# Performance work log

Measured on AMD Instinct MI355X. Metric: run time of the kernel, lower is better.

Reference implementation:

```python
import jax, jax.numpy as jnp
import numpy as np

N, L = 5, 2097152
WIDTH = 11  # max_pool1d kernel width in the original


def setup_inputs() -> dict:
    key = jax.random.key(0)
    k1, k2 = jax.random.split(key)
    rppg = jax.random.normal(k1, (N, L), dtype=jnp.float32)
    ppg = jax.random.normal(k2, (N, L), dtype=jnp.float32)
    return {"rppg": rppg, "ppg": ppg, "fs": 30, "epoch": 15}


def _normalize(x):
    # normalize_torch: per-signal standardization
    mu = x.mean(axis=1, keepdims=True)
    sd = x.std(axis=1, keepdims=True)
    return (x - mu) / sd


def _window_max(x, width):
    # sliding max over centered window of `width`, same padding (-inf pad)
    return jax.lax.reduce_window(x, -jnp.inf, jax.lax.max,
                                 (1, width), (1, 1),
                                 [(0, 0), (width // 2, width // 2)])


def _mean_hr(x, fs):
    # A position p is a 'nice peak' iff max_pool argmax at p equals p,
    # i.e. x[p] is the max of its own centered window (ties have measure 0
    # for continuous signals). unique()+masking collapses to this mask.
    w = _window_max(x, WIDTH)
    m1 = x == w                                            # [N, L] peak mask
    npk = m1.sum(axis=1, keepdims=True).astype(x.dtype)
    mean_pk = (x * m1).sum(axis=1, keepdims=True) / npk    # mean of peak values
    m = m1 & (x > mean_pk / 2)                             # amplitude-filtered peaks
    idx = jnp.arange(x.shape[1])
    vals = jnp.where(m, idx, -1)
    # previous peak index strictly before p (fixed-shape replacement for diff
    # over a variable-length peak index list)
    prev = jnp.pad(jax.lax.cummax(vals, axis=1)[:, :-1], ((0, 0), (1, 0)),
                   constant_values=-1)
    valid = m & (prev >= 0)                                # one entry per inter-peak gap
    gaps = (idx[None, :] - prev).astype(x.dtype)
    inv = jnp.where(valid, 1.0 / gaps, 0.0)
    # mean(60 / (gap / fs)) = 60 * fs * mean(1 / gap)
    return (60.0 * fs) * inv.sum(axis=1) / valid.sum(axis=1).astype(x.dtype)


def reference(rppg, ppg, fs, epoch):
    ppg = _normalize(ppg.reshape(N, -1))
    rppg = _normalize(rppg.reshape(N, -1))
    ppg_hr = _mean_hr(ppg, fs)
    rppg_hr = _mean_hr(rppg, fs)
    # hr_score = mean_i |ppg_hr - rppg_hr| / ppg_hr  (peak_score is computed
    # in the original but not returned)
    return jnp.mean(jnp.abs(ppg_hr - rppg_hr) / ppg_hr)
```

## Files before the change

kernel.cpp:

```cpp
#include <hip/hip_runtime.h>
#include <math.h>

namespace {

constexpr int LNUM = 2097152;
constexpr int NROW = 5;
constexpr int NSER = 10;
constexpr int TPB = 256;
constexpr int EPL = 16;
constexpr int CHUNK = TPB * EPL;
constexpr int CPR = LNUM / CHUNK;
constexpr int NBLK = NSER * CPR;

struct Agg { int first; int last; int c; double s; };

__device__ __forceinline__ Agg combine(const Agg& a, const Agg& b) {
  Agg r;
  r.first = (a.first >= 0) ? a.first : b.first;
  r.last  = (b.last >= 0) ? b.last : a.last;
  r.s = a.s + b.s;
  r.c = a.c + b.c;
  if (a.last >= 0 && b.first >= 0) {
    r.s += 1.0 / (double)(b.first - a.last);
    r.c += 1;
  }
  return r;
}

__device__ __forceinline__ void window16(const float* __restrict__ x, int s,
                                         float X[26], float w[16]) {
  const float4* q = reinterpret_cast<const float4*>(x + s);
  float4 f0 = q[0], f1 = q[1], f2 = q[2], f3 = q[3];
  X[5] = f0.x;  X[6] = f0.y;  X[7] = f0.z;  X[8] = f0.w;
  X[9] = f1.x;  X[10] = f1.y; X[11] = f1.z; X[12] = f1.w;
  X[13] = f2.x; X[14] = f2.y; X[15] = f2.z; X[16] = f2.w;
  X[17] = f3.x; X[18] = f3.y; X[19] = f3.z; X[20] = f3.w;
#pragma unroll
  for (int j = 0; j < 5; ++j) X[j] = __shfl_up(X[16 + j], 1);
#pragma unroll
  for (int j = 0; j < 5; ++j) X[21 + j] = __shfl_down(X[5 + j], 1);
  const int lane = threadIdx.x & 63;
  if (lane == 0) {
#pragma unroll
    for (int j = 0; j < 5; ++j) {
      int g = s - 5 + j;
      X[j] = (g >= 0) ? x[g] : -INFINITY;
    }
  }
  if (lane == 63) {
#pragma unroll
    for (int j = 0; j < 5; ++j) {
      int g = s + 16 + j;
      X[21 + j] = (g < LNUM) ? x[g] : -INFINITY;
    }
  }
  float m2[25];
#pragma unroll
  for (int i = 0; i < 25; ++i) m2[i] = fmaxf(X[i], X[i + 1]);
  float m4[23];
#pragma unroll
  for (int i = 0; i < 23; ++i) m4[i] = fmaxf(m2[i], m2[i + 2]);
  float m8[19];
#pragma unroll
  for (int i = 0; i < 19; ++i) m8[i] = fmaxf(m4[i], m4[i + 4]);
#pragma unroll
  for (int t = 0; t < 16; ++t) w[t] = fmaxf(m8[t], m8[t + 3]);
}

__device__ __forceinline__ const float* row_ptr(const float* rppg,
                                                const float* ppg, int rw) {
  return (rw < NROW) ? rppg + (size_t)rw * LNUM
                     : ppg + (size_t)(rw - NROW) * LNUM;
}

__global__ __launch_bounds__(TPB) void stats_kernel(
    const float* __restrict__ rppg, const float* __restrict__ ppg,
    double* __restrict__ psum, double* __restrict__ ppk,
    int* __restrict__ pnpk) {
  const int bid = blockIdx.x;
  const int rw = bid >> 9;
  const int chunk = bid & (CPR - 1);
  const float* x = row_ptr(rppg, ppg, rw);
  const int lane = threadIdx.x & 63;
  const int wid = threadIdx.x >> 6;
  const int s = chunk * CHUNK + wid * (64 * EPL) + lane * EPL;

  float X[26], w[16];
  window16(x, s, X, w);

  double tsum = 0.0, tpk = 0.0;
  int tn = 0;
#pragma unroll
  for (int t = 0; t < 16; ++t) {
    float v = X[5 + t];
    tsum += (double)v;
    if (v == w[t]) { tpk += (double)v; ++tn; }
  }
#pragma unroll
  for (int off = 32; off > 0; off >>= 1) {
    tsum += __shfl_down(tsum, off);
    tpk  += __shfl_down(tpk, off);
    tn   += __shfl_down(tn, off);
  }

  __shared__ double wsum[4], wpk[4];
  __shared__ int wn[4];
  if (lane == 0) { wsum[wid] = tsum; wpk[wid] = tpk; wn[wid] = tn; }
  __syncthreads();
  if (threadIdx.x == 0) {
    psum[bid] = wsum[0] + wsum[1] + wsum[2] + wsum[3];
    ppk[bid]  = wpk[0] + wpk[1] + wpk[2] + wpk[3];
    pnpk[bid] = wn[0] + wn[1] + wn[2] + wn[3];
  }
}

__global__ __launch_bounds__(TPB) void thresh_kernel(
    const double* __restrict__ psum, const double* __restrict__ ppk,
    const int* __restrict__ pnpk, double* __restrict__ thr) {
  const int r = blockIdx.x;
  const int t = threadIdx.x;
  const int lane = t & 63;
  const int wid = t >> 6;
  double s0 = psum[r * CPR + t] + psum[r * CPR + t + 256];
  double p0 = ppk[r * CPR + t] + ppk[r * CPR + t + 256];
  int n0 = pnpk[r * CPR + t] + pnpk[r * CPR + t + 256];
#pragma unroll
  for (int off = 32; off > 0; off >>= 1) {
    s0 += __shfl_down(s0, off);
    p0 += __shfl_down(p0, off);
    n0 += __shfl_down(n0, off);
  }
  __shared__ double ws[4], wp[4];
  __shared__ int wn[4];
  if (lane == 0) { ws[wid] = s0; wp[wid] = p0; wn[wid] = n0; }
  __syncthreads();
  if (t == 0) {
    double S = ws[0] + ws[1] + ws[2] + ws[3];
    double P = wp[0] + wp[1] + wp[2] + wp[3];
    double Nn = (double)(wn[0] + wn[1] + wn[2] + wn[3]);
    thr[r] = 0.5 * (S / (double)LNUM + P / Nn);
  }
}

__global__ __launch_bounds__(TPB) void gap_kernel(
    const float* __restrict__ rppg, const float* __restrict__ ppg,
    const double* __restrict__ thr,
    int* __restrict__ cfirst, int* __restrict__ clast,
    double* __restrict__ csum, int* __restrict__ ccnt) {
  const int bid = blockIdx.x;
  const int rw = bid >> 9;
  const int chunk = bid & (CPR - 1);
  const float* x = row_ptr(rppg, ppg, rw);
  const float th = (float)thr[rw];
  const int lane = threadIdx.x & 63;
  const int wid = threadIdx.x >> 6;
  const int s = chunk * CHUNK + wid * (64 * EPL) + lane * EPL;

  float X[26], w[16];
  window16(x, s, X, w);

  Agg a; a.first = -1; a.last = -1; a.c = 0; a.s = 0.0;
#pragma unroll
  for (int t = 0; t < 16; ++t) {
    float v = X[5 + t];
    if (v == w[t] && v > th) {
      int p = s + t;
      if (a.last >= 0) { a.s += 1.0 / (double)(p - a.last); ++a.c; }
      else a.first = p;
      a.last = p;
    }
  }
#pragma unroll
  for (int off = 1; off < 64; off <<= 1) {
    Agg b;
    b.first = __shfl_down(a.first, off);
    b.last  = __shfl_down(a.last, off);
    b.c     = __shfl_down(a.c, off);
    b.s     = __shfl_down(a.s, off);
    a = combine(a, b);
  }

  __shared__ Agg waggs[4];
  if (lane == 0) waggs[wid] = a;
  __syncthreads();
  if (threadIdx.x == 0) {
    Agg r = waggs[0];
    r = combine(r, waggs[1]);
    r = combine(r, waggs[2]);
    r = combine(r, waggs[3]);
    cfirst[bid] = r.first; clast[bid] = r.last;
    csum[bid] = r.s; ccnt[bid] = r.c;
  }
}

__global__ __launch_bounds__(TPB) void final_kernel(
    const int* __restrict__ cfirst, const int* __restrict__ clast,
    const double* __restrict__ csum, const int* __restrict__ ccnt,
    const int* __restrict__ fsp, float* __restrict__ out) {
  __shared__ Agg waggs[4];
  __shared__ double shr[NSER];
  const int t = threadIdx.x;
  const int lane = t & 63;
  const int wid = t >> 6;
  for (int r = 0; r < NSER; ++r) {
    const int i0 = r * CPR + 2 * t;
    Agg a0; a0.first = cfirst[i0];     a0.last = clast[i0];
    a0.c = ccnt[i0];                   a0.s = csum[i0];
    Agg a1; a1.first = cfirst[i0 + 1]; a1.last = clast[i0 + 1];
    a1.c = ccnt[i0 + 1];               a1.s = csum[i0 + 1];
    a0 = combine(a0, a1);
#pragma unroll
    for (int off = 1; off < 64; off <<= 1) {
      Agg b;
      b.first = __shfl_down(a0.first, off);
      b.last  = __shfl_down(a0.last, off);
      b.c     = __shfl_down(a0.c, off);
      b.s     = __shfl_down(a0.s, off);
      a0 = combine(a0, b);
    }
    if (lane == 0) waggs[wid] = a0;
    __syncthreads();
    if (t == 0) {
      Agg rr = waggs[0];
      rr = combine(rr, waggs[1]);
      rr = combine(rr, waggs[2]);
      rr = combine(rr, waggs[3]);
      shr[r] = 60.0 * (double)fsp[0] * rr.s / (double)rr.c;
    }
    __syncthreads();
  }
  if (t == 0) {
    double acc = 0.0;
    for (int r = 0; r < NROW; ++r)
      acc += fabs(shr[NROW + r] - shr[r]) / shr[NROW + r];
    out[0] = (float)(acc / (double)NROW);
  }
}

}

extern "C" void kernel_launch(void* const* d_in, const int* in_sizes, int n_in,
                              void* d_out, int out_size, void* d_ws, size_t ws_size,
                              hipStream_t stream) {
  const float* rppg = (const float*)d_in[0];
  const float* ppg  = (const float*)d_in[1];
  const int* fsp    = (const int*)d_in[2];
  float* out        = (float*)d_out;
  char* ws          = (char*)d_ws;

  double* psum   = (double*)(ws);
  double* ppk    = (double*)(ws + 40960);
  int*    pnpk   = (int*)(ws + 81920);
  double* csum   = (double*)(ws + 102400);
  int*    cfirst = (int*)(ws + 143360);
  int*    clast  = (int*)(ws + 163840);
  int*    ccnt   = (int*)(ws + 184320);
  double* thr    = (double*)(ws + 204800);

  stats_kernel<<<NBLK, TPB, 0, stream>>>(rppg, ppg, psum, ppk, pnpk);
  thresh_kernel<<<NSER, TPB, 0, stream>>>(psum, ppk, pnpk, thr);
  gap_kernel<<<NBLK, TPB, 0, stream>>>(rppg, ppg, thr, cfirst, clast, csum, ccnt);
  final_kernel<<<1, TPB, 0, stream>>>(cfirst, clast, csum, ccnt, fsp, out);
  (void)in_sizes; (void)n_in; (void)out_size; (void)ws_size;
}
```

Baseline: 154.4 us.

## Restructure per-lane window loads to coalesced float4 strips with wave-level loops

Replaces the 16-element-per-lane window with a 4-element float4 per lane, iterated 4 times per warp segment, so consecutive lanes read consecutive 16-byte pieces. Halo values now come via shuffles of distance 1 and 2, plus edge loads. The gap kernel performs a full wave reduction of peak aggregates per iteration and combines the results serially. The aim is better load coalescing, at the cost of more shuffle and reduction work.

Result: slower. 185.6 us (+20.2%).

```diff
diff --git a/kernel.cpp b/kernel.cpp
--- a/kernel.cpp
+++ b/kernel.cpp
@@ -7,10 +7,10 @@
 constexpr int NROW = 5;
 constexpr int NSER = 10;
 constexpr int TPB = 256;
-constexpr int EPL = 16;
-constexpr int CHUNK = TPB * EPL;
+constexpr int CHUNK = 4096;
 constexpr int CPR = LNUM / CHUNK;
 constexpr int NBLK = NSER * CPR;
+constexpr int KIT = 4;
 
 struct Agg { int first; int last; int c; double s; };
 
@@ -27,50 +27,56 @@
   return r;
 }
 
-__device__ __forceinline__ void window16(const float* __restrict__ x, int s,
-                                         float X[26], float w[16]) {
-  const float4* q = reinterpret_cast<const float4*>(x + s);
-  float4 f0 = q[0], f1 = q[1], f2 = q[2], f3 = q[3];
-  X[5] = f0.x;  X[6] = f0.y;  X[7] = f0.z;  X[8] = f0.w;
-  X[9] = f1.x;  X[10] = f1.y; X[11] = f1.z; X[12] = f1.w;
-  X[13] = f2.x; X[14] = f2.y; X[15] = f2.z; X[16] = f2.w;
-  X[17] = f3.x; X[18] = f3.y; X[19] = f3.z; X[20] = f3.w;
-#pragma unroll
-  for (int j = 0; j < 5; ++j) X[j] = __shfl_up(X[16 + j], 1);
-#pragma unroll
-  for (int j = 0; j < 5; ++j) X[21 + j] = __shfl_down(X[5 + j], 1);
-  const int lane = threadIdx.x & 63;
-  if (lane == 0) {
-#pragma unroll
-    for (int j = 0; j < 5; ++j) {
-      int g = s - 5 + j;
-      X[j] = (g >= 0) ? x[g] : -INFINITY;
-    }
-  }
-  if (lane == 63) {
-#pragma unroll
-    for (int j = 0; j < 5; ++j) {
-      int g = s + 16 + j;
-      X[21 + j] = (g < LNUM) ? x[g] : -INFINITY;
-    }
-  }
-  float m2[25];
-#pragma unroll
-  for (int i = 0; i < 25; ++i) m2[i] = fmaxf(X[i], X[i + 1]);
-  float m4[23];
-#pragma unroll
-  for (int i = 0; i < 23; ++i) m4[i] = fmaxf(m2[i], m2[i + 2]);
-  float m8[19];
-#pragma unroll
-  for (int i = 0; i < 19; ++i) m8[i] = fmaxf(m4[i], m4[i + 4]);
-#pragma unroll
-  for (int t = 0; t < 16; ++t) w[t] = fmaxf(m8[t], m8[t + 3]);
-}
-
 __device__ __forceinline__ const float* row_ptr(const float* rppg,
                                                 const float* ppg, int rw) {
   return (rw < NROW) ? rppg + (size_t)rw * LNUM
                      : ppg + (size_t)(rw - NROW) * LNUM;
+}
+
+__device__ __forceinline__ void window4(const float* __restrict__ x, int p0,
+                                        float X[4], float w[4]) {
+  const float4 f = *reinterpret_cast<const float4*>(x + p0);
+  X[0] = f.x; X[1] = f.y; X[2] = f.z; X[3] = f.w;
+  float Y[14];
+  Y[5] = X[0]; Y[6] = X[1]; Y[7] = X[2]; Y[8] = X[3];
+  Y[1] = __shfl_up(X[0], 1);  Y[2] = __shfl_up(X[1], 1);
+  Y[3] = __shfl_up(X[2], 1);  Y[4] = __shfl_up(X[3], 1);
+  Y[0] = __shfl_up(X[3], 2);
+  Y[9] = __shfl_down(X[0], 1);  Y[10] = __shfl_down(X[1], 1);
+  Y[11] = __shfl_down(X[2], 1); Y[12] = __shfl_down(X[3], 1);
+  Y[13] = __shfl_down(X[0], 2);
+  const int lane = threadIdx.x & 63;
+  if (lane == 0) {
+#pragma unroll
+    for (int j = 0; j < 5; ++j) {
+      int g = p0 - 5 + j;
+      Y[j] = (g >= 0) ? x[g] : -INFINITY;
+    }
+  } else if (lane == 1) {
+    int g = p0 - 5;
+    Y[0] = (g >= 0) ? x[g] : -INFINITY;
+  }
+  if (lane == 63) {
+#pragma unroll
+    for (int j = 0; j < 5; ++j) {
+      int g = p0 + 4 + j;
+      Y[9 + j] = (g < LNUM) ? x[g] : -INFINITY;
+    }
+  } else if (lane == 62) {
+    int g = p0 + 8;
+    Y[13] = (g < LNUM) ? x[g] : -INFINITY;
+  }
+  float m2[13];
+#pragma unroll
+  for (int i = 0; i < 13; ++i) m2[i] = fmaxf(Y[i], Y[i + 1]);
+  float m4[11];
+#pragma unroll
+  for (int i = 0; i < 11; ++i) m4[i] = fmaxf(m2[i], m2[i + 2]);
+  float m8[7];
+#pragma unroll
+  for (int i = 0; i < 7; ++i) m8[i] = fmaxf(m4[i], m4[i + 4]);
+#pragma unroll
+  for (int t = 0; t < 4; ++t) w[t] = fmaxf(m8[t], m8[t + 3]);
 }
 
 __global__ __launch_bounds__(TPB) void stats_kernel(
@@ -83,18 +89,19 @@
   const float* x = row_ptr(rppg, ppg, rw);
   const int lane = threadIdx.x & 63;
   const int wid = threadIdx.x >> 6;
-  const int s = chunk * CHUNK + wid * (64 * EPL) + lane * EPL;
-
-  float X[26], w[16];
-  window16(x, s, X, w);
+  const int segbase = chunk * CHUNK + wid * 1024;
 
   double tsum = 0.0, tpk = 0.0;
   int tn = 0;
-#pragma unroll
-  for (int t = 0; t < 16; ++t) {
-    float v = X[5 + t];
-    tsum += (double)v;
-    if (v == w[t]) { tpk += (double)v; ++tn; }
+  for (int k = 0; k < KIT; ++k) {
+    const int p0 = segbase + k * 256 + 4 * lane;
+    float X[4], w[4];
+    window4(x, p0, X, w);
+#pragma unroll
+    for (int t = 0; t < 4; ++t) {
+      tsum += (double)X[t];
+      if (X[t] == w[t]) { tpk += (double)X[t]; ++tn; }
+    }
   }
 #pragma unroll
   for (int off = 32; off > 0; off >>= 1) {
@@ -102,7 +109,6 @@
     tpk  += __shfl_down(tpk, off);
     tn   += __shfl_down(tn, off);
   }
-
   __shared__ double wsum[4], wpk[4];
   __shared__ int wn[4];
   if (lane == 0) { wsum[wid] = tsum; wpk[wid] = tpk; wn[wid] = tn; }
@@ -154,34 +160,42 @@
   const float th = (float)thr[rw];
   const int lane = threadIdx.x & 63;
   const int wid = threadIdx.x >> 6;
-  const int s = chunk * CHUNK + wid * (64 * EPL) + lane * EPL;
-
-  float X[26], w[16];
-  window16(x, s, X, w);
-
-  Agg a; a.first = -1; a.last = -1; a.c = 0; a.s = 0.0;
-#pragma unroll
-  for (int t = 0; t < 16; ++t) {
-    float v = X[5 + t];
-    if (v == w[t] && v > th) {
-      int p = s + t;
-      if (a.last >= 0) { a.s += 1.0 / (double)(p - a.last); ++a.c; }
-      else a.first = p;
-      a.last = p;
-    }
-  }
-#pragma unroll
-  for (int off = 1; off < 64; off <<= 1) {
-    Agg b;
-    b.first = __shfl_down(a.first, off);
-    b.last  = __shfl_down(a.last, off);
-    b.c     = __shfl_down(a.c, off);
-    b.s     = __shfl_down(a.s, off);
-    a = combine(a, b);
+  const int segbase = chunk * CHUNK + wid * 1024;
+
+  Agg wacc; wacc.first = -1; wacc.last = -1; wacc.c = 0; wacc.s = 0.0;
+  for (int k = 0; k < KIT; ++k) {
+    const int p0 = segbase + k * 256 + 4 * lane;
+    float X[4], w[4];
+    window4(x, p0, X, w);
+    Agg a; a.first = -1; a.last = -1; a.c = 0; a.s = 0.0;
+#pragma unroll
+    for (int t = 0; t < 4; ++t) {
+      if (X[t] == w[t] && X[t] > th) {
+        int p = p0 + t;
+        if (a.last >= 0) { a.s += 1.0 / (double)(p - a.last); ++a.c; }
+        else a.first = p;
+        a.last = p;
+      }
+    }
+#pragma unroll
+    for (int off = 1; off < 64; off <<= 1) {
+      Agg b;
+      b.first = __shfl_down(a.first, off);
+      b.last  = __shfl_down(a.last, off);
+      b.c     = __shfl_down(a.c, off);
+      b.s     = __shfl_down(a.s, off);
+      a = combine(a, b);
+    }
+    Agg t0;
+    t0.first = __shfl(a.first, 0);
+    t0.last  = __shfl(a.last, 0);
+    t0.c     = __shfl(a.c, 0);
+    t0.s     = __shfl(a.s, 0);
+    wacc = combine(wacc, t0);
   }
 
   __shared__ Agg waggs[4];
-  if (lane == 0) waggs[wid] = a;
+  if (lane == 0) waggs[wid] = wacc;
   __syncthreads();
   if (threadIdx.x == 0) {
     Agg r = waggs[0];
```
